# Optimization experiments

Hardware: AMD Instinct MI355X
Metric: run time of the kernel (lower is better)

Reference implementation:

```python
import jax, jax.numpy as jnp
import numpy as np

WIN = 7
NUM_HEADS = 4
HEAD_DIM = 32  # 128 / 4


def _relative_position_index(win=WIN):
    coords = np.stack(np.meshgrid(np.arange(win), np.arange(win), indexing='ij'))  # [2,w,w]
    coords = coords.reshape(2, -1)  # [2, w*w]
    rel = coords[:, :, None] - coords[:, None, :]  # [2, ws, ws]
    rel = rel.transpose(1, 2, 0)  # [ws, ws, 2]
    idx = (rel[..., 0] + win - 1) * (2 * win - 1) + (rel[..., 1] + win - 1)
    return jnp.asarray(idx, dtype=jnp.int32)  # [49, 49]


def setup_inputs() -> dict:
    key = jax.random.key(0)
    ks = jax.random.split(key, 6)
    B, S, D = 4096, WIN * WIN, 128
    nW = 64  # windows per image
    return {
        'hidden_states': jax.random.normal(ks[0], (B, S, D), dtype=jnp.float32),
        'attention_mask': jnp.zeros((nW, S, S), dtype=jnp.float32),
        'Wq': jax.random.normal(ks[1], (D, D), dtype=jnp.float32) * 0.02,
        'bq': jnp.zeros((D,), dtype=jnp.float32),
        'Wk': jax.random.normal(ks[2], (D, D), dtype=jnp.float32) * 0.02,
        'bk': jnp.zeros((D,), dtype=jnp.float32),
        'Wv': jax.random.normal(ks[3], (D, D), dtype=jnp.float32) * 0.02,
        'bv': jnp.zeros((D,), dtype=jnp.float32),
        'bias_table': jax.random.normal(ks[4], ((2 * WIN - 1) ** 2, NUM_HEADS), dtype=jnp.float32) * 0.02,
    }


def reference(hidden_states, attention_mask, Wq, bq, Wk, bk, Wv, bv, bias_table):
    B, S, D = hidden_states.shape
    H, Dh = NUM_HEADS, HEAD_DIM

    def heads(x):  # [B,S,D] -> [B,H,S,Dh]
        return x.reshape(B, S, H, Dh).transpose(0, 2, 1, 3)

    q = heads(hidden_states @ Wq + bq)
    k = heads(hidden_states @ Wk + bk)
    v = heads(hidden_states @ Wv + bv)

    scores = jnp.einsum('bhqd,bhkd->bhqk', q, k) / np.sqrt(Dh).astype(np.float32)

    idx = _relative_position_index()  # [S,S] int32 constant
    rel_bias = bias_table[idx]  # [S,S,H]
    scores = scores + rel_bias.transpose(2, 0, 1)[None]  # [B,H,S,S]

    nW = attention_mask.shape[0]
    scores = scores.reshape(B // nW, nW, H, S, S) + attention_mask[None, :, None]
    scores = scores.reshape(B, H, S, S)

    probs = jax.nn.softmax(scores, axis=-1)
    ctx = jnp.einsum('bhqk,bhkd->bhqd', probs, v)
    return ctx.transpose(0, 2, 1, 3).reshape(B, S, D)
```

## Files before the change

kernel.cpp:

```cpp
#include <hip/hip_runtime.h>
#include <hip/hip_bf16.h>

#define S49 49
#define D128 128
#define NH 4

typedef __attribute__((ext_vector_type(8))) short short8;
typedef __attribute__((ext_vector_type(4))) float f32x4;

__device__ __forceinline__ unsigned short f2b(float x){
  unsigned u = __builtin_bit_cast(unsigned, x);
  return (unsigned short)((u + 0x7fffu + ((u>>16)&1u)) >> 16);
}
__device__ __forceinline__ unsigned pk2(float a, float b){
  __hip_bfloat162 h = __float22bfloat162_rn(float2{a, b});
  unsigned u; __builtin_memcpy(&u, &h, 4);
  return u;
}
__device__ __forceinline__ int swz256i(int row, int col){
  return row*128 + ((((col>>3) ^ (row&15)) << 3) | (col&7));
}
__device__ __forceinline__ int swz128i(int row, int col){
  return row*64 + ((((col>>3) ^ (row&7)) << 3) | (col&7));
}

__global__ void prep_wt(const float* __restrict__ Wq, const float* __restrict__ Wk,
                        const float* __restrict__ Wv, unsigned short* __restrict__ wt){
  int e = blockIdx.x*256 + threadIdx.x;
  if (e >= 3*128*128) return;
  int mat = e >> 14, rem = e & 16383, n = rem >> 7, k = rem & 127;
  const float* W = (mat==0) ? Wq : ((mat==1) ? Wk : Wv);
  wt[e] = f2b(W[k*128 + n]);
}

__global__ void prep_comb(const float* __restrict__ mask, const float* __restrict__ bt,
                          float4* __restrict__ comb4, int nW){
  int e = blockIdx.x*256 + threadIdx.x;
  if (e >= nW*NH*S49*16) return;
  int ln = e & 15; int t = e >> 4;
  int i = t % S49; t /= S49;
  int h = t & (NH-1); int w = t / NH;
  const float* mrow = mask + ((size_t)w*S49 + i)*S49;
  int ri = i/7, ci = i - ri*7;
  const float L2E = 1.4426950408889634f;
  float v[4];
  #pragma unroll
  for (int nt = 0; nt < 4; ++nt){
    int j = nt*16 + ln;
    if (j < S49){
      int rj = j/7, cj = j - rj*7;
      int idx = (ri - rj + 6)*13 + (ci - cj + 6);
      v[nt] = (mrow[j] + bt[idx*NH + h]) * L2E;
    } else v[nt] = -1e30f;
  }
  float4 o; o.x = v[0]; o.y = v[1]; o.z = v[2]; o.w = v[3];
  comb4[e] = o;
}

__global__ __launch_bounds__(512, 4) void swin_attn(
    const float* __restrict__ hs,
    const float* __restrict__ bq, const float* __restrict__ bk,
    const float* __restrict__ bv,
    const float4* __restrict__ comb4,
    const unsigned short* __restrict__ wt, float* __restrict__ out, int nW){

  __shared__ __align__(16) unsigned short lds[29056];
  unsigned short* hs_s = lds;
  unsigned short* q_s  = lds + 6272;
  unsigned short* k_s  = lds + 12544;
  unsigned short* vt_s = lds + 18816;
  unsigned short* pext = lds + 27008;

  const int b = blockIdx.x;
  const int tid = threadIdx.x;
  const int wave = tid >> 6, lane = tid & 63;
  const int lg = lane >> 4, ln = lane & 15;
  unsigned short* pp = (wave < 6) ? (hs_s + wave*1024) : (pext + (wave-6)*1024);

  const float* hsb = hs + (size_t)b * (S49*D128);
  #pragma unroll
  for (int it = 0; it < 4; ++it) {
    int u = tid + it*512;
    if (u < S49*32) {
      int row = u >> 5, c = u & 31;
      float4 f = *(const float4*)(hsb + row*128 + c*4);
      uint2 o; o.x = pk2(f.x, f.y); o.y = pk2(f.z, f.w);
      *(uint2*)&hs_s[swz256i(row, c*4)] = o;
    }
  }
  #pragma unroll
  for (int it = 0; it < 4; ++it) {
    int u = tid + it*512;
    if (u < 128*15) {
      int r = u/15, c = 49 + (u - r*15);
      vt_s[swz128i(r, c)] = 0;
    }
  }
  __syncthreads();

  {
    const int ntb = wave*16;
    short8 a[3][4];
    #pragma unroll
    for (int mat = 0; mat < 3; ++mat)
      #pragma unroll
      for (int ks = 0; ks < 4; ++ks)
        a[mat][ks] = *(const short8*)&wt[(mat<<14) + (ntb+ln)*128 + ks*32 + lg*8];
    float4 bias_q = *(const float4*)&bq[ntb + 4*lg];
    float4 bias_k = *(const float4*)&bk[ntb + 4*lg];
    float4 bias_v = *(const float4*)&bv[ntb + 4*lg];
    #pragma unroll
    for (int mt = 0; mt < 4; ++mt) {
      const int mb = (mt<3) ? mt*16 : 33;
      short8 bh[4];
      #pragma unroll
      for (int ks = 0; ks < 4; ++ks)
        bh[ks] = *(const short8*)&hs_s[swz256i(mb+ln, ks*32 + lg*8)];
      #pragma unroll
      for (int mat = 0; mat < 3; ++mat) {
        f32x4 acc = {0.f,0.f,0.f,0.f};
        #pragma unroll
        for (int ks = 0; ks < 4; ++ks)
          acc = __builtin_amdgcn_mfma_f32_16x16x32_bf16(a[mat][ks], bh[ks], acc, 0,0,0);
        const int m = mb + ln;
        const int nb = ntb + 4*lg;
        if (mat == 0) {
          uint2 o; o.x = pk2(acc[0]+bias_q.x, acc[1]+bias_q.y);
                   o.y = pk2(acc[2]+bias_q.z, acc[3]+bias_q.w);
          *(uint2*)&q_s[swz256i(m, nb)] = o;
        } else if (mat == 1) {
          uint2 o; o.x = pk2(acc[0]+bias_k.x, acc[1]+bias_k.y);
                   o.y = pk2(acc[2]+bias_k.z, acc[3]+bias_k.w);
          *(uint2*)&k_s[swz256i(m, nb)] = o;
        } else {
          vt_s[swz128i(nb+0, m)] = f2b(acc[0]+bias_v.x);
          vt_s[swz128i(nb+1, m)] = f2b(acc[1]+bias_v.y);
          vt_s[swz128i(nb+2, m)] = f2b(acc[2]+bias_v.z);
          vt_s[swz128i(nb+3, m)] = f2b(acc[3]+bias_v.w);
        }
      }
    }
  }
  __syncthreads();

  const float C1 = 0.17677669529663687f * 1.4426950408889634f;
  const int w = b % nW;
  const int rt = wave & 3, hp = wave >> 1 >> 1;
  const int mbw = (rt<3) ? rt*16 : 33;
  const short8 ones = {16256,16256,16256,16256,16256,16256,16256,16256};

  #pragma unroll
  for (int hh = 0; hh < 2; ++hh) {
    const int h = hp*2 + hh;
    float4 cb[4];
    #pragma unroll
    for (int r = 0; r < 4; ++r)
      cb[r] = comb4[((size_t)(w*NH + h)*S49 + mbw + 4*lg + r)*16 + ln];

    short8 aq = *(const short8*)&q_s[swz256i(mbw+ln, h*32 + lg*8)];
    short8 kb[4];
    #pragma unroll
    for (int nt = 0; nt < 4; ++nt)
      kb[nt] = *(const short8*)&k_s[swz256i(nt*16+ln, h*32 + lg*8)];
    if (ln != 0) kb[3] = short8{0,0,0,0,0,0,0,0};
    f32x4 s[4];
    __builtin_amdgcn_s_setprio(1);
    #pragma unroll
    for (int nt = 0; nt < 4; ++nt) {
      f32x4 z = {0.f,0.f,0.f,0.f};
      s[nt] = __builtin_amdgcn_mfma_f32_16x16x32_bf16(aq, kb[nt], z, 0,0,0);
    }
    __builtin_amdgcn_s_setprio(0);

    #pragma unroll
    for (int r = 0; r < 4; ++r) {
      float cbv[4] = {cb[r].x, cb[r].y, cb[r].z, cb[r].w};
      #pragma unroll
      for (int nt = 0; nt < 4; ++nt) {
        float e = exp2f(fmaf(s[nt][r], C1, cbv[nt]));
        pp[swz128i(4*lg + r, nt*16 + ln)] = f2b(e);
      }
    }

    short8 ap0 = *(const short8*)&pp[swz128i(ln, lg*8)];
    short8 ap1 = *(const short8*)&pp[swz128i(ln, 32 + lg*8)];
    f32x4 sacc = {0.f,0.f,0.f,0.f};
    __builtin_amdgcn_s_setprio(1);
    sacc = __builtin_amdgcn_mfma_f32_16x16x32_bf16(ap0, ones, sacc, 0,0,0);
    sacc = __builtin_amdgcn_mfma_f32_16x16x32_bf16(ap1, ones, sacc, 0,0,0);
    __builtin_amdgcn_s_setprio(0);
    float inv[4];
    #pragma unroll
    for (int r = 0; r < 4; ++r) inv[r] = __builtin_amdgcn_rcpf(sacc[r]);

    #pragma unroll
    for (int nt = 0; nt < 2; ++nt) {
      const int vr = h*32 + nt*16 + ln;
      short8 bv0 = *(const short8*)&vt_s[swz128i(vr, lg*8)];
      short8 bv1 = *(const short8*)&vt_s[swz128i(vr, 32 + lg*8)];
      f32x4 acc = {0.f,0.f,0.f,0.f};
      __builtin_amdgcn_s_setprio(1);
      acc = __builtin_amdgcn_mfma_f32_16x16x32_bf16(ap0, bv0, acc, 0,0,0);
      acc = __builtin_amdgcn_mfma_f32_16x16x32_bf16(ap1, bv1, acc, 0,0,0);
      __builtin_amdgcn_s_setprio(0);
      const int mr = mbw + 4*lg;
      #pragma unroll
      for (int r = 0; r < 4; ++r)
        out[((size_t)b*S49 + mr + r)*D128 + vr] = acc[r]*inv[r];
    }
  }
}

extern "C" void kernel_launch(void* const* d_in, const int* in_sizes, int n_in,
                              void* d_out, int out_size, void* d_ws, size_t ws_size,
                              hipStream_t stream){
  const float* hs  = (const float*)d_in[0];
  const float* msk = (const float*)d_in[1];
  const float* Wq  = (const float*)d_in[2];
  const float* bq  = (const float*)d_in[3];
  const float* Wk  = (const float*)d_in[4];
  const float* bk  = (const float*)d_in[5];
  const float* Wv  = (const float*)d_in[6];
  const float* bv  = (const float*)d_in[7];
  const float* bt  = (const float*)d_in[8];
  unsigned short* wt = (unsigned short*)d_ws;
  float4* comb4 = (float4*)((char*)d_ws + 98304);
  float* out = (float*)d_out;
  const int B  = in_sizes[0] / (S49*D128);
  const int nW = in_sizes[1] / (S49*S49);
  prep_wt<<<dim3((3*128*128 + 255)/256), dim3(256), 0, stream>>>(Wq, Wk, Wv, wt);
  prep_comb<<<dim3((nW*NH*S49*16 + 255)/256), dim3(256), 0, stream>>>(msk, bt, comb4, nW);
  swin_attn<<<dim3(B), dim3(512), 0, stream>>>(hs, bq, bk, bv, comb4, wt, out, nW);
}
```

Before: 102.1 us.

## Shrink LDS footprint with compact padded layouts to raise occupancy

Replaces the 64-wide swizzled V^T and probability tiles with compact row strides (56 and 52 elements), zero-padding only the columns the MFMA needs and masking tail fragments in registers. This cuts the block's shared memory so launch bounds can target 6 blocks per CU instead of 4. The bias/mask loads for both heads are hoisted before the barrier so their latency overlaps the projection. The unswizzled strides may cause LDS bank conflicts, and the higher occupancy target constrains registers, which could lead to spills.

```diff
diff --git a/kernel.cpp b/kernel.cpp
--- a/kernel.cpp
+++ b/kernel.cpp
@@ -6,6 +6,7 @@
 #define NH 4
 
 typedef __attribute__((ext_vector_type(8))) short short8;
+typedef __attribute__((ext_vector_type(4))) short short4v;
 typedef __attribute__((ext_vector_type(4))) float f32x4;
 
 __device__ __forceinline__ unsigned short f2b(float x){
@@ -19,9 +20,6 @@
 }
 __device__ __forceinline__ int swz256i(int row, int col){
   return row*128 + ((((col>>3) ^ (row&15)) << 3) | (col&7));
-}
-__device__ __forceinline__ int swz128i(int row, int col){
-  return row*64 + ((((col>>3) ^ (row&7)) << 3) | (col&7));
 }
 
 __global__ void prep_wt(const float* __restrict__ Wq, const float* __restrict__ Wk,
@@ -57,25 +55,25 @@
   comb4[e] = o;
 }
 
-__global__ __launch_bounds__(512, 4) void swin_attn(
+__global__ __launch_bounds__(512, 6) void swin_attn(
     const float* __restrict__ hs,
     const float* __restrict__ bq, const float* __restrict__ bk,
     const float* __restrict__ bv,
     const float4* __restrict__ comb4,
     const unsigned short* __restrict__ wt, float* __restrict__ out, int nW){
 
-  __shared__ __align__(16) unsigned short lds[29056];
+  __shared__ __align__(16) unsigned short lds[26832];
   unsigned short* hs_s = lds;
   unsigned short* q_s  = lds + 6272;
   unsigned short* k_s  = lds + 12544;
   unsigned short* vt_s = lds + 18816;
-  unsigned short* pext = lds + 27008;
+  unsigned short* pext = lds + 25984;
 
   const int b = blockIdx.x;
   const int tid = threadIdx.x;
   const int wave = tid >> 6, lane = tid & 63;
   const int lg = lane >> 4, ln = lane & 15;
-  unsigned short* pp = (wave < 6) ? (hs_s + wave*1024) : (pext + (wave-6)*1024);
+  unsigned short* pp = (wave < 7) ? (hs_s + wave*832) : pext;
 
   const float* hsb = hs + (size_t)b * (S49*D128);
   #pragma unroll
@@ -89,14 +87,18 @@
     }
   }
   #pragma unroll
-  for (int it = 0; it < 4; ++it) {
+  for (int it = 0; it < 2; ++it) {
     int u = tid + it*512;
-    if (u < 128*15) {
-      int r = u/15, c = 49 + (u - r*15);
-      vt_s[swz128i(r, c)] = 0;
+    if (u < 128*7) {
+      int r = u/7, c = 49 + (u - r*7);
+      vt_s[r*56 + c] = 0;
     }
   }
   __syncthreads();
+
+  const int w = b % nW;
+  const int rt = wave & 3, hp = wave >> 2;
+  const int mbw = (rt<3) ? rt*16 : 33;
 
   {
     const int ntb = wave*16;
@@ -133,29 +135,31 @@
                    o.y = pk2(acc[2]+bias_k.z, acc[3]+bias_k.w);
           *(uint2*)&k_s[swz256i(m, nb)] = o;
         } else {
-          vt_s[swz128i(nb+0, m)] = f2b(acc[0]+bias_v.x);
-          vt_s[swz128i(nb+1, m)] = f2b(acc[1]+bias_v.y);
-          vt_s[swz128i(nb+2, m)] = f2b(acc[2]+bias_v.z);
-          vt_s[swz128i(nb+3, m)] = f2b(acc[3]+bias_v.w);
+          vt_s[(nb+0)*56 + m] = f2b(acc[0]+bias_v.x);
+          vt_s[(nb+1)*56 + m] = f2b(acc[1]+bias_v.y);
+          vt_s[(nb+2)*56 + m] = f2b(acc[2]+bias_v.z);
+          vt_s[(nb+3)*56 + m] = f2b(acc[3]+bias_v.w);
         }
       }
     }
   }
+
+  float4 cb[2][4];
+  #pragma unroll
+  for (int hh = 0; hh < 2; ++hh)
+    #pragma unroll
+    for (int r = 0; r < 4; ++r)
+      cb[hh][r] = comb4[((size_t)(w*NH + hp*2 + hh)*S49 + mbw + 4*lg + r)*16 + ln];
+
   __syncthreads();
 
   const float C1 = 0.17677669529663687f * 1.4426950408889634f;
-  const int w = b % nW;
-  const int rt = wave & 3, hp = wave >> 1 >> 1;
-  const int mbw = (rt<3) ? rt*16 : 33;
   const short8 ones = {16256,16256,16256,16256,16256,16256,16256,16256};
+  const short4v z4 = {0,0,0,0};
 
   #pragma unroll
   for (int hh = 0; hh < 2; ++hh) {
     const int h = hp*2 + hh;
-    float4 cb[4];
-    #pragma unroll
-    for (int r = 0; r < 4; ++r)
-      cb[r] = comb4[((size_t)(w*NH + h)*S49 + mbw + 4*lg + r)*16 + ln];
 
     short8 aq = *(const short8*)&q_s[swz256i(mbw+ln, h*32 + lg*8)];
     short8 kb[4];
@@ -174,16 +178,24 @@
 
     #pragma unroll
     for (int r = 0; r < 4; ++r) {
-      float cbv[4] = {cb[r].x, cb[r].y, cb[r].z, cb[r].w};
+      float cbv[4] = {cb[hh][r].x, cb[hh][r].y, cb[hh][r].z, cb[hh][r].w};
       #pragma unroll
       for (int nt = 0; nt < 4; ++nt) {
         float e = exp2f(fmaf(s[nt][r], C1, cbv[nt]));
-        pp[swz128i(4*lg + r, nt*16 + ln)] = f2b(e);
+        if (nt < 3 || ln < 4)
+          pp[(4*lg + r)*52 + nt*16 + ln] = f2b(e);
       }
     }
 
-    short8 ap0 = *(const short8*)&pp[swz128i(ln, lg*8)];
-    short8 ap1 = *(const short8*)&pp[swz128i(ln, 32 + lg*8)];
+    short4v a0 = *(const short4v*)&pp[ln*52 + lg*8];
+    short4v a1 = *(const short4v*)&pp[ln*52 + lg*8 + 4];
+    short8 ap0 = __builtin_shufflevector(a0, a1, 0,1,2,3,4,5,6,7);
+    short4v b0 = *(const short4v*)&pp[ln*52 + 32 + lg*8];
+    short4v b1 = *(const short4v*)&pp[ln*52 + 36 + lg*8];
+    if (lg >= 2) b1 = z4;
+    if (lg == 3) b0 = z4;
+    short8 ap1 = __builtin_shufflevector(b0, b1, 0,1,2,3,4,5,6,7);
+
     f32x4 sacc = {0.f,0.f,0.f,0.f};
     __builtin_amdgcn_s_setprio(1);
     sacc = __builtin_amdgcn_mfma_f32_16x16x32_bf16(ap0, ones, sacc, 0,0,0);
@@ -196,8 +208,9 @@
     #pragma unroll
     for (int nt = 0; nt < 2; ++nt) {
       const int vr = h*32 + nt*16 + ln;
-      short8 bv0 = *(const short8*)&vt_s[swz128i(vr, lg*8)];
-      short8 bv1 = *(const short8*)&vt_s[swz128i(vr, 32 + lg*8)];
+      short8 bv0 = *(const short8*)&vt_s[vr*56 + lg*8];
+      short8 bv1 = {0,0,0,0,0,0,0,0};
+      if (lg < 3) bv1 = *(const short8*)&vt_s[vr*56 + 32 + lg*8];
       f32x4 acc = {0.f,0.f,0.f,0.f};
       __builtin_amdgcn_s_setprio(1);
       acc = __builtin_amdgcn_mfma_f32_16x16x32_bf16(ap0, bv0, acc, 0,0,0);
```

Measured after the change: 243.8 us. 2.39x slower.
